# Kernel optimization log

Hardware: AMD Instinct MI355X
Metric: run time of the kernel (lower is better)

The kernel has to match this reference:

```python
import jax, jax.numpy as jnp
import numpy as np

LENGTH = 128
BATCH = 256
MARGIN = 1.0
BONUS = 1000.0  # constraint bump applied to chart cells
NCELLS = LENGTH * (LENGTH + 1) // 2
NCONSTR = 8


def _offsets(length):
    off = np.zeros(length, dtype=np.int64)
    for lvl in range(1, length):
        off[lvl] = off[lvl - 1] + (length - (lvl - 1))
    return off

OFF = _offsets(LENGTH)


def _level_child_indices(length):
    # For each level: flat chart indices of left/right children, shape (L, N)
    idx = {}
    for level in range(1, length):
        L = length - level
        pos = np.arange(L)[:, None]
        n = np.arange(level)[None, :]
        l_idx = OFF[n] + pos                      # left child span (pos, width n)
        r_idx = OFF[level - 1 - n] + pos + n + 1  # right child span
        idx[level] = (jnp.asarray(l_idx), jnp.asarray(r_idx))
    return idx

IDX = _level_child_indices(LENGTH)


def _score_offsets(length):
    soff, acc = {}, 0
    for level in range(1, length):
        soff[level] = acc
        acc += (length - level) * level
    return soff, acc

SOFF, TOTAL = _score_offsets(LENGTH)


def setup_inputs():
    key = jax.random.key(0)
    k1, k2 = jax.random.split(key)
    scores = jax.random.normal(k1, (BATCH, TOTAL), dtype=jnp.float32)
    # constrained spans at level >= 1 (original skips level <= 0)
    constraint_pos = jax.random.randint(k2, (BATCH, NCONSTR), LENGTH, NCELLS, dtype=jnp.int32)
    return {"scores": scores, "constraint_pos": constraint_pos}


def _cky(scores, chart):
    # max-plus semiring inside DP, level by level over the triangular chart
    B = chart.shape[0]
    for level in range(1, LENGTH):
        L = LENGTH - level
        N = level
        l_idx, r_idx = IDX[level]
        ls = chart[:, l_idx]                                     # (B, L, N)
        rs = chart[:, r_idx]                                     # (B, L, N)
        xs = scores[:, SOFF[level]:SOFF[level] + L * N].reshape(B, L, N)
        best = jnp.max(ls + rs + xs, axis=2)                     # (B, L)
        off = int(OFF[level])
        chart = chart.at[:, off:off + L].add(best)
    return chart[:, -1]                                          # (B,) root scores


def reference(scores, constraint_pos):
    B = scores.shape[0]
    zero_chart = jnp.zeros((B, NCELLS), dtype=scores.dtype)
    rows = jnp.arange(B)[:, None]
    constr_chart = zero_chart.at[rows, constraint_pos].set(BONUS)
    subtract = jnp.full((B,), BONUS * constraint_pos.shape[1], dtype=scores.dtype)
    constr_s = _cky(scores, constr_chart) - subtract
    pred_s = _cky(scores, zero_chart)
    mask = (jnp.abs(pred_s - constr_s) >= 0.001).astype(scores.dtype)
    hinge = jnp.maximum(MARGIN + pred_s - constr_s, 0.0) * mask
    msum = mask.sum()
    return jnp.where(msum > 0.1, hinge.sum() / jnp.maximum(msum, 1.0), hinge.sum())
```

## Files before the change

### kernel.cpp

```cpp
#include <hip/hip_runtime.h>
#include <hip/hip_bf16.h>
#include <math.h>

#define LEN 128
#define NCELLS 8256
#define TOTAL 349504
#define NCONSTR 8
#define BONUS 1000.0f
#define NT 512

__device__ __forceinline__ void level_barrier() {
    __builtin_amdgcn_sched_barrier(0);
    asm volatile("s_waitcnt lgkmcnt(0)\n\ts_barrier" ::: "memory");
    __builtin_amdgcn_sched_barrier(0);
}

__device__ __forceinline__ float dpp_xor1_max(float v) {
    int r = __builtin_amdgcn_update_dpp(0, __float_as_int(v), 0xB1, 0xF, 0xF, true);
    return fmaxf(v, __int_as_float(r));
}
__device__ __forceinline__ float dpp_xor2_max(float v) {
    int r = __builtin_amdgcn_update_dpp(0, __float_as_int(v), 0x4E, 0xF, 0xF, true);
    return fmaxf(v, __int_as_float(r));
}

template<int LG>
__device__ __forceinline__ void redmax2(float& a, float& b) {
    #pragma unroll
    for (int mm = (1 << LG) >> 1; mm >= 4; mm >>= 1) {
        a = fmaxf(a, __shfl_xor(a, mm));
        b = fmaxf(b, __shfl_xor(b, mm));
    }
    if constexpr (LG >= 2) { a = dpp_xor2_max(a); b = dpp_xor2_max(b); }
    if constexpr (LG >= 1) { a = dpp_xor1_max(a); b = dpp_xor1_max(b); }
}

template<int LG, int LG2, int JM, int JM2>
__device__ __forceinline__ void lstep(const int level, int& soff,
        const float* __restrict__ g, float2* __restrict__ chart,
        float (&rcur)[16], float (&rnxt)[16], const int tid)
{
    const int N = level;
    const int L = LEN - level;
    constexpr int T = 1 << LG;
    const int pos = tid >> LG;
    const int sub = tid & (T - 1);
    const int soff_n = soff + L * N;

    if constexpr (LG2 >= 0) {
        constexpr int T2 = 1 << LG2;
        const int N2 = level + 1;
        const int L2 = L - 1;
        const int pos2 = tid >> LG2;
        const int sub2 = tid & (T2 - 1);
        if (pos2 < L2) {
            const float* __restrict__ gp = g + soff_n + pos2 * N2 + sub2;
            #pragma unroll
            for (int j = 0; j < JM2; j++) {
                if (sub2 + j * T2 < N2) rnxt[j] = gp[j * T2];
            }
        }
    }

    float bp = -INFINITY, bc = -INFINITY;
    if (pos < L) {
        const int jml = (N - sub + T - 1) >> LG;
        float2 lv[JM], rv[JM];
        float  xs[JM];
        #pragma unroll
        for (int j = 0; j < JM; j++) {
            const int n = sub + j * T;
            const int m = level - 1 - n;
            const bool v = (j < jml);
            const int l_idx = ((n * (257 - n)) >> 1) + pos;
            int r_idx = ((m * (257 - m)) >> 1) + pos + n + 1;
            r_idx = v ? r_idx : 0;
            lv[j] = chart[l_idx];
            rv[j] = chart[r_idx];
            xs[j] = v ? rcur[j] : -INFINITY;
        }
        #pragma unroll
        for (int j = 0; j < JM; j++) {
            bp = fmaxf(bp, lv[j].x + rv[j].x + xs[j]);
            bc = fmaxf(bc, lv[j].y + rv[j].y + xs[j]);
        }
    }
    redmax2<LG>(bp, bc);
    if (pos < L && sub == 0) {
        const int q = ((level * (257 - level)) >> 1) + pos;
        float2 c = chart[q];
        c.x += bp;
        c.y += bc;
        chart[q] = c;
    }
    level_barrier();
    soff = soff_n;
}

template<int K>
__device__ __forceinline__ void seg4(int& soff, const float* __restrict__ g,
        float2* __restrict__ chart, float (&rA)[16], float (&rB)[16], const int tid)
{
    const int l0 = 4 * K - 3;
    #pragma unroll 1
    for (int l = l0; l < l0 + 4; l += 2) {
        lstep<2, 2, K, K + 1>(l,     soff, g, chart, rA, rB, tid);
        lstep<2, 2, K, K + 1>(l + 1, soff, g, chart, rB, rA, tid);
    }
}

__global__ __launch_bounds__(NT)
void cky_fused_kernel(const float* __restrict__ scores,
                      const int* __restrict__ cpos,
                      float* __restrict__ ws)
{
    __shared__ float2 chart[NCELLS];

    const int b   = blockIdx.x;
    const int tid = threadIdx.x;
    const float* __restrict__ g = scores + (size_t)b * TOTAL;

    float rA[16], rB[16];

    {
        const int pos = tid >> 2;
        const int sub = tid & 3;
        if (pos < 127 && sub == 0) rA[0] = g[pos];
    }
    int cp = -1;
    if (tid < NCONSTR) cp = cpos[b * NCONSTR + tid];

    for (int i = tid; i < NCELLS; i += NT) chart[i] = make_float2(0.f, 0.f);
    level_barrier();
    if (tid < NCONSTR) chart[cp].y = BONUS;
    level_barrier();

    int soff = 0;

    seg4<1>(soff, g, chart, rA, rB, tid);
    seg4<2>(soff, g, chart, rA, rB, tid);
    seg4<3>(soff, g, chart, rA, rB, tid);
    seg4<4>(soff, g, chart, rA, rB, tid);
    seg4<5>(soff, g, chart, rA, rB, tid);
    seg4<6>(soff, g, chart, rA, rB, tid);
    seg4<7>(soff, g, chart, rA, rB, tid);
    seg4<8>(soff, g, chart, rA, rB, tid);
    seg4<9>(soff, g, chart, rA, rB, tid);
    seg4<10>(soff, g, chart, rA, rB, tid);
    seg4<11>(soff, g, chart, rA, rB, tid);
    seg4<12>(soff, g, chart, rA, rB, tid);
    seg4<13>(soff, g, chart, rA, rB, tid);
    seg4<14>(soff, g, chart, rA, rB, tid);
    seg4<15>(soff, g, chart, rA, rB, tid);
    lstep<2,2,16,16>(61, soff, g, chart, rA, rB, tid);
    lstep<2,2,16,16>(62, soff, g, chart, rB, rA, tid);
    lstep<2,3,16,8>(63, soff, g, chart, rA, rB, tid);
    lstep<3,3,8,9>(64, soff, g, chart, rB, rA, tid);
    #pragma unroll 1
    for (int l = 65; l < 72; l += 2) {
        lstep<3,3,9,10>(l,     soff, g, chart, rA, rB, tid);
        lstep<3,3,9,10>(l + 1, soff, g, chart, rB, rA, tid);
    }
    #pragma unroll 1
    for (int l = 73; l < 80; l += 2) {
        lstep<3,3,10,11>(l,     soff, g, chart, rA, rB, tid);
        lstep<3,3,10,11>(l + 1, soff, g, chart, rB, rA, tid);
    }
    #pragma unroll 1
    for (int l = 81; l < 88; l += 2) {
        lstep<3,3,11,12>(l,     soff, g, chart, rA, rB, tid);
        lstep<3,3,11,12>(l + 1, soff, g, chart, rB, rA, tid);
    }
    #pragma unroll 1
    for (int l = 89; l < 94; l += 2) {
        lstep<3,3,12,12>(l,     soff, g, chart, rA, rB, tid);
        lstep<3,3,12,12>(l + 1, soff, g, chart, rB, rA, tid);
    }
    lstep<3,4,12,6>(95, soff, g, chart, rA, rB, tid);
    lstep<4,4,6,7>(96, soff, g, chart, rB, rA, tid);
    #pragma unroll 1
    for (int l = 97; l < 110; l += 2) {
        lstep<4,4,7,7>(l,     soff, g, chart, rA, rB, tid);
        lstep<4,4,7,7>(l + 1, soff, g, chart, rB, rA, tid);
    }
    lstep<4,5,7,4>(111, soff, g, chart, rA, rB, tid);
    lstep<5,5,4,4>(112, soff, g, chart, rB, rA, tid);
    #pragma unroll 1
    for (int l = 113; l < 118; l += 2) {
        lstep<5,5,4,4>(l,     soff, g, chart, rA, rB, tid);
        lstep<5,5,4,4>(l + 1, soff, g, chart, rB, rA, tid);
    }
    lstep<5,6,4,2>(119, soff, g, chart, rA, rB, tid);
    lstep<6,6,2,2>(120, soff, g, chart, rB, rA, tid);
    #pragma unroll 1
    for (int l = 121; l < 126; l += 2) {
        lstep<6,6,2,2>(l,     soff, g, chart, rA, rB, tid);
        lstep<6,6,2,2>(l + 1, soff, g, chart, rB, rA, tid);
    }
    lstep<6,-1,2,2>(127, soff, g, chart, rA, rB, tid);

    if (tid == 0) {
        const float2 f = chart[NCELLS - 1];
        const float pred   = f.x;
        const float constr = f.y - BONUS * NCONSTR;
        const float diff   = pred - constr;
        const float mask   = (fabsf(diff) >= 0.001f) ? 1.f : 0.f;
        const float hinge  = fmaxf(1.0f + diff, 0.f) * mask;
        atomicAdd(ws + 0, hinge);
        atomicAdd(ws + 1, mask);
    }
}

__global__ void final_kernel(const float* __restrict__ ws, float* __restrict__ out) {
    const float h = ws[0];
    const float m = ws[1];
    out[0] = (m > 0.1f) ? (h / fmaxf(m, 1.f)) : h;
}

extern "C" void kernel_launch(void* const* d_in, const int* in_sizes, int n_in,
                              void* d_out, int out_size, void* d_ws, size_t ws_size,
                              hipStream_t stream) {
    const float* scores = (const float*)d_in[0];
    const int*   cpos   = (const int*)d_in[1];
    float* out = (float*)d_out;
    float* ws  = (float*)d_ws;

    hipMemsetAsync(ws, 0, 2 * sizeof(float), stream);
    cky_fused_kernel<<<dim3(256), dim3(NT), 0, stream>>>(scores, cpos, ws);
    final_kernel<<<dim3(1), dim3(1), 0, stream>>>(ws, out);
}
```

Measured before the change: 142.1 us.

## Stage per-level scores into double-buffered LDS via global_load_lds

Replaces per-thread register prefetch of next-level scores with coalesced 16-byte async global-to-LDS copies into two ping-pong shared buffers. Compute now reads scores from LDS using a padded aligned offset. This aims to make global loads fully coalesced and cut register pressure, but each level barrier now waits on vmcnt(0), so every level stalls on the prefetch. It also adds about 35KB of LDS use and an extra LDS read per element.

```diff
diff --git a/kernel.cpp b/kernel.cpp
--- a/kernel.cpp
+++ b/kernel.cpp
@@ -8,10 +8,19 @@
 #define NCONSTR 8
 #define BONUS 1000.0f
 #define NT 512
+#define SBUF 4480
+
+typedef __attribute__((address_space(1))) const unsigned int guint;
+typedef __attribute__((address_space(3))) unsigned int luint;
 
 __device__ __forceinline__ void level_barrier() {
     __builtin_amdgcn_sched_barrier(0);
     asm volatile("s_waitcnt lgkmcnt(0)\n\ts_barrier" ::: "memory");
+    __builtin_amdgcn_sched_barrier(0);
+}
+__device__ __forceinline__ void drain_barrier() {
+    __builtin_amdgcn_sched_barrier(0);
+    asm volatile("s_waitcnt vmcnt(0) lgkmcnt(0)\n\ts_barrier" ::: "memory");
     __builtin_amdgcn_sched_barrier(0);
 }
 
@@ -23,7 +32,6 @@
     int r = __builtin_amdgcn_update_dpp(0, __float_as_int(v), 0x4E, 0xF, 0xF, true);
     return fmaxf(v, __int_as_float(r));
 }
-
 template<int LG>
 __device__ __forceinline__ void redmax2(float& a, float& b) {
     #pragma unroll
@@ -35,10 +43,26 @@
     if constexpr (LG >= 1) { a = dpp_xor1_max(a); b = dpp_xor1_max(b); }
 }
 
-template<int LG, int LG2, int JM, int JM2>
+__device__ __forceinline__ void stage(const float* __restrict__ g, int soff,
+                                      int LN, float* __restrict__ dst, int tid)
+{
+    const int chunks = (LN + 258) >> 8;
+    int astart = soff & ~3;
+    const int amax = TOTAL - (chunks << 8);
+    astart = (astart < amax) ? astart : amax;
+    const int w = tid >> 6;
+    const float* src = g + astart + ((tid & 63) << 2);
+    #pragma unroll 1
+    for (int c = w; c < chunks; c += 8) {
+        __builtin_amdgcn_global_load_lds((guint*)(src + (c << 8)),
+                                         (luint*)(dst + (c << 8)), 16, 0, 0);
+    }
+}
+
+template<int LG, int JM, bool STG>
 __device__ __forceinline__ void lstep(const int level, int& soff,
         const float* __restrict__ g, float2* __restrict__ chart,
-        float (&rcur)[16], float (&rnxt)[16], const int tid)
+        const float* __restrict__ sbc, float* __restrict__ sbn, const int tid)
 {
     const int N = level;
     const int L = LEN - level;
@@ -47,24 +71,24 @@
     const int sub = tid & (T - 1);
     const int soff_n = soff + L * N;
 
-    if constexpr (LG2 >= 0) {
-        constexpr int T2 = 1 << LG2;
-        const int N2 = level + 1;
-        const int L2 = L - 1;
-        const int pos2 = tid >> LG2;
-        const int sub2 = tid & (T2 - 1);
-        if (pos2 < L2) {
-            const float* __restrict__ gp = g + soff_n + pos2 * N2 + sub2;
-            #pragma unroll
-            for (int j = 0; j < JM2; j++) {
-                if (sub2 + j * T2 < N2) rnxt[j] = gp[j * T2];
-            }
-        }
+    if constexpr (STG) {
+        stage(g, soff_n, (L - 1) * (N + 1), sbn, tid);
+    }
+
+    int pad;
+    {
+        const int LN = L * N;
+        const int chk = (LN + 258) >> 8;
+        int ast = soff & ~3;
+        const int am = TOTAL - (chk << 8);
+        ast = (ast < am) ? ast : am;
+        pad = soff - ast;
     }
 
     float bp = -INFINITY, bc = -INFINITY;
     if (pos < L) {
         const int jml = (N - sub + T - 1) >> LG;
+        const float* xrow = sbc + pad + pos * N + sub;
         float2 lv[JM], rv[JM];
         float  xs[JM];
         #pragma unroll
@@ -77,7 +101,8 @@
             r_idx = v ? r_idx : 0;
             lv[j] = chart[l_idx];
             rv[j] = chart[r_idx];
-            xs[j] = v ? rcur[j] : -INFINITY;
+            const float xl = xrow[j * T];
+            xs[j] = v ? xl : -INFINITY;
         }
         #pragma unroll
         for (int j = 0; j < JM; j++) {
@@ -93,19 +118,20 @@
         c.y += bc;
         chart[q] = c;
     }
-    level_barrier();
+    drain_barrier();
     soff = soff_n;
 }
 
 template<int K>
 __device__ __forceinline__ void seg4(int& soff, const float* __restrict__ g,
-        float2* __restrict__ chart, float (&rA)[16], float (&rB)[16], const int tid)
+        float2* __restrict__ chart, float* __restrict__ sb0,
+        float* __restrict__ sb1, const int tid)
 {
     const int l0 = 4 * K - 3;
     #pragma unroll 1
     for (int l = l0; l < l0 + 4; l += 2) {
-        lstep<2, 2, K, K + 1>(l,     soff, g, chart, rA, rB, tid);
-        lstep<2, 2, K, K + 1>(l + 1, soff, g, chart, rB, rA, tid);
+        lstep<2, K, true>(l,     soff, g, chart, sb1, sb0, tid);
+        lstep<2, K, true>(l + 1, soff, g, chart, sb0, sb1, tid);
     }
 }
 
@@ -115,89 +141,87 @@
                       float* __restrict__ ws)
 {
     __shared__ float2 chart[NCELLS];
+    __shared__ float  sbuf[2][SBUF];
 
     const int b   = blockIdx.x;
     const int tid = threadIdx.x;
     const float* __restrict__ g = scores + (size_t)b * TOTAL;
-
-    float rA[16], rB[16];
-
-    {
-        const int pos = tid >> 2;
-        const int sub = tid & 3;
-        if (pos < 127 && sub == 0) rA[0] = g[pos];
-    }
-    int cp = -1;
+    float* __restrict__ sb0 = &sbuf[0][0];
+    float* __restrict__ sb1 = &sbuf[1][0];
+
+    stage(g, 0, 127, sb1, tid);
+
+    int cp = 0;
     if (tid < NCONSTR) cp = cpos[b * NCONSTR + tid];
 
     for (int i = tid; i < NCELLS; i += NT) chart[i] = make_float2(0.f, 0.f);
-    level_barrier();
+    drain_barrier();
     if (tid < NCONSTR) chart[cp].y = BONUS;
     level_barrier();
 
     int soff = 0;
 
-    seg4<1>(soff, g, chart, rA, rB, tid);
-    seg4<2>(soff, g, chart, rA, rB, tid);
-    seg4<3>(soff, g, chart, rA, rB, tid);
-    seg4<4>(soff, g, chart, rA, rB, tid);
-    seg4<5>(soff, g, chart, rA, rB, tid);
-    seg4<6>(soff, g, chart, rA, rB, tid);
-    seg4<7>(soff, g, chart, rA, rB, tid);
-    seg4<8>(soff, g, chart, rA, rB, tid);
-    seg4<9>(soff, g, chart, rA, rB, tid);
-    seg4<10>(soff, g, chart, rA, rB, tid);
-    seg4<11>(soff, g, chart, rA, rB, tid);
-    seg4<12>(soff, g, chart, rA, rB, tid);
-    seg4<13>(soff, g, chart, rA, rB, tid);
-    seg4<14>(soff, g, chart, rA, rB, tid);
-    seg4<15>(soff, g, chart, rA, rB, tid);
-    lstep<2,2,16,16>(61, soff, g, chart, rA, rB, tid);
-    lstep<2,2,16,16>(62, soff, g, chart, rB, rA, tid);
-    lstep<2,3,16,8>(63, soff, g, chart, rA, rB, tid);
-    lstep<3,3,8,9>(64, soff, g, chart, rB, rA, tid);
+    seg4<1>(soff, g, chart, sb0, sb1, tid);
+    seg4<2>(soff, g, chart, sb0, sb1, tid);
+    seg4<3>(soff, g, chart, sb0, sb1, tid);
+    seg4<4>(soff, g, chart, sb0, sb1, tid);
+    seg4<5>(soff, g, chart, sb0, sb1, tid);
+    seg4<6>(soff, g, chart, sb0, sb1, tid);
+    seg4<7>(soff, g, chart, sb0, sb1, tid);
+    seg4<8>(soff, g, chart, sb0, sb1, tid);
+    seg4<9>(soff, g, chart, sb0, sb1, tid);
+    seg4<10>(soff, g, chart, sb0, sb1, tid);
+    seg4<11>(soff, g, chart, sb0, sb1, tid);
+    seg4<12>(soff, g, chart, sb0, sb1, tid);
+    seg4<13>(soff, g, chart, sb0, sb1, tid);
+    seg4<14>(soff, g, chart, sb0, sb1, tid);
+    seg4<15>(soff, g, chart, sb0, sb1, tid);
+    lstep<2,16,true>(61, soff, g, chart, sb1, sb0, tid);
+    lstep<2,16,true>(62, soff, g, chart, sb0, sb1, tid);
+    lstep<2,16,true>(63, soff, g, chart, sb1, sb0, tid);
+    lstep<3,8,true> (64, soff, g, chart, sb0, sb1, tid);
     #pragma unroll 1
     for (int l = 65; l < 72; l += 2) {
-        lstep<3,3,9,10>(l,     soff, g, chart, rA, rB, tid);
-        lstep<3,3,9,10>(l + 1, soff, g, chart, rB, rA, tid);
+        lstep<3,9,true>(l,     soff, g, chart, sb1, sb0, tid);
+        lstep<3,9,true>(l + 1, soff, g, chart, sb0, sb1, tid);
     }
     #pragma unroll 1
     for (int l = 73; l < 80; l += 2) {
-        lstep<3,3,10,11>(l,     soff, g, chart, rA, rB, tid);
-        lstep<3,3,10,11>(l + 1, soff, g, chart, rB, rA, tid);
+        lstep<3,10,true>(l,     soff, g, chart, sb1, sb0, tid);
+        lstep<3,10,true>(l + 1, soff, g, chart, sb0, sb1, tid);
     }
     #pragma unroll 1
     for (int l = 81; l < 88; l += 2) {
-        lstep<3,3,11,12>(l,     soff, g, chart, rA, rB, tid);
-        lstep<3,3,11,12>(l + 1, soff, g, chart, rB, rA, tid);
+        lstep<3,11,true>(l,     soff, g, chart, sb1, sb0, tid);
+        lstep<3,11,true>(l + 1, soff, g, chart, sb0, sb1, tid);
     }
     #pragma unroll 1
     for (int l = 89; l < 94; l += 2) {
-        lstep<3,3,12,12>(l,     soff, g, chart, rA, rB, tid);
-        lstep<3,3,12,12>(l + 1, soff, g, chart, rB, rA, tid);
-    }
-    lstep<3,4,12,6>(95, soff, g, chart, rA, rB, tid);
-    lstep<4,4,6,7>(96, soff, g, chart, rB, rA, tid);
+        lstep<3,12,true>(l,     soff, g, chart, sb1, sb0, tid);
+        lstep<3,12,true>(l + 1, soff, g, chart, sb0, sb1, tid);
+    }
+    lstep<3,12,true>(95, soff, g, chart, sb1, sb0, tid);
+    lstep<4,6,true> (96, soff, g, chart, sb0, sb1, tid);
     #pragma unroll 1
     for (int l = 97; l < 110; l += 2) {
-        lstep<4,4,7,7>(l,     soff, g, chart, rA, rB, tid);
-        lstep<4,4,7,7>(l + 1, soff, g, chart, rB, rA, tid);
-    }
-    lstep<4,5,7,4>(111, soff, g, chart, rA, rB, tid);
-    lstep<5,5,4,4>(112, soff, g, chart, rB, rA, tid);
+        lstep<4,7,true>(l,     soff, g, chart, sb1, sb0, tid);
+        lstep<4,7,true>(l + 1, soff, g, chart, sb0, sb1, tid);
+    }
+    lstep<4,7,true>(111, soff, g, chart, sb1, sb0, tid);
+    lstep<5,4,true>(112, soff, g, chart, sb0, sb1, tid);
     #pragma unroll 1
     for (int l = 113; l < 118; l += 2) {
-        lstep<5,5,4,4>(l,     soff, g, chart, rA, rB, tid);
-        lstep<5,5,4,4>(l + 1, soff, g, chart, rB, rA, tid);
-    }
-    lstep<5,6,4,2>(119, soff, g, chart, rA, rB, tid);
-    lstep<6,6,2,2>(120, soff, g, chart, rB, rA, tid);
+        lstep<5,4,true>(l,     soff, g, chart, sb1, sb0, tid);
+        lstep<5,4,true>(l + 1, soff, g, chart, sb0, sb1, tid);
+    }
+    lstep<5,4,true>(119, soff, g, chart, sb1, sb0, tid);
+    lstep<6,2,true>(120, soff, g, chart, sb0, sb1, tid);
     #pragma unroll 1
     for (int l = 121; l < 126; l += 2) {
-        lstep<6,6,2,2>(l,     soff, g, chart, rA, rB, tid);
-        lstep<6,6,2,2>(l + 1, soff, g, chart, rB, rA, tid);
-    }
-    lstep<6,-1,2,2>(127, soff, g, chart, rA, rB, tid);
+        lstep<6,2,true>(l,     soff, g, chart, sb1, sb0, tid);
+        lstep<6,2,true>(l + 1, soff, g, chart, sb0, sb1, tid);
+    }
+    lstep<6,2,false>(127, soff, g, chart, sb1, sb0, tid);
 
     if (tid == 0) {
         const float2 f = chart[NCELLS - 1];
```

Measured after the change: 148.7 us. +4.7%, slower.
